# Kernel optimization log

Hardware: AMD Instinct MI355X
Metric: run time of the kernel (lower is better)

The kernel has to match this reference:

```python
import jax, jax.numpy as jnp
import numpy as np

E = 8          # num_experts
G = 4          # n_expert_groups
LG = 2         # n_limited_groups
TOPK = 2
ROUTE_SCALE = 1.0


def _grouped_mm(x, w, counts):
    """Grouped GEMM: contiguous groups of rows of x (sizes=counts) hit w[e]. Matches torch._grouped_mm."""
    counts = counts.astype(jnp.int32)
    if hasattr(jax.lax, 'ragged_dot'):
        return jax.lax.ragged_dot(x, w, counts)
    # fallback: expert id per row via searchsorted on offsets, one-hot dispatch
    offs = jnp.cumsum(counts)
    eid = jnp.searchsorted(offs, jnp.arange(x.shape[0]), side='right')
    oh = jax.nn.one_hot(eid, w.shape[0], dtype=x.dtype)
    return jnp.einsum('nd,ne,edh->nh', x, oh, w)


def setup_inputs() -> dict:
    key = jax.random.key(0)
    ks = jax.random.split(key, 8)
    bs, slen, dim, hid, shid = 2, 2048, 1024, 512, 1024
    std = 0.02
    return {
        'x': jax.random.normal(ks[0], (bs, slen, dim), jnp.float32),
        'w_gate': jax.random.normal(ks[1], (E, dim), jnp.float32) * std,
        'w1': jax.random.normal(ks[2], (E, dim, hid), jnp.float32) * std,
        'w2': jax.random.normal(ks[3], (E, hid, dim), jnp.float32) * std,
        'w3': jax.random.normal(ks[4], (E, dim, hid), jnp.float32) * std,
        'sw1': jax.random.normal(ks[5], (shid, dim), jnp.float32) * std,
        'sw2': jax.random.normal(ks[6], (dim, shid), jnp.float32) * std,
        'sw3': jax.random.normal(ks[7], (shid, dim), jnp.float32) * std,
        'expert_bias': jnp.zeros((E,), jnp.float32),
    }


def reference(x, w_gate, w1, w2, w3, sw1, sw2, sw3, expert_bias):
    bs, slen, dim = x.shape
    xf = x.reshape(-1, dim)                       # [N, dim]
    N = xf.shape[0]

    # ---- Gate (group-limited top-k routing) ----
    logits = xf @ w_gate.T                        # [N, E]
    scores = jax.nn.softmax(logits.astype(jnp.float32), axis=-1)
    original = scores
    s = (scores + expert_bias).reshape(N, G, E // G)
    # expert_bias is not None branch: group score = sum of top-2 in group
    group_scores = jax.lax.top_k(s, 2)[0].sum(-1)            # [N, G]
    top_groups = jax.lax.top_k(group_scores, LG)[1]          # [N, LG]
    keep = jnp.zeros((N, G), bool).at[jnp.arange(N)[:, None], top_groups].set(True)
    masked = jnp.where(keep[:, :, None], s, -jnp.inf).reshape(N, E)
    topk_idx = jax.lax.top_k(masked, TOPK)[1]                # [N, k]
    weights = (jnp.take_along_axis(original, topk_idx, axis=1) * ROUTE_SCALE).astype(x.dtype)
    counts = jnp.bincount(topk_idx.reshape(-1), length=E)    # histc equivalent

    # ---- dispatch (faithful to source: gather rows of x by expert ids) ----
    flat_idx = topk_idx.reshape(-1)                          # [N*k], values in [0, E)
    routed_in = xf[flat_idx]                                 # [N*k, dim]
    # score_before_experts = True
    routed_in = (routed_in.astype(jnp.float32) * weights.reshape(-1, 1)).astype(x.dtype)

    # ---- grouped experts: SwiGLU via grouped GEMM ----
    h = jax.nn.silu(_grouped_mm(routed_in, w1, counts)) * _grouped_mm(routed_in, w3, counts)
    routed_out = _grouped_mm(h, w2, counts)                  # [N*k, dim]

    # ---- shared experts (SwiGLU FFN) + combine (faithful scatter by expert ids) ----
    shared = (jax.nn.silu(xf @ sw1.T) * (xf @ sw3.T)) @ sw2.T
    out = shared.at[flat_idx].add(routed_out)
    return out.reshape(bs, slen, dim)
```

## Files before the change

### kernel.cpp

```cpp
#include <hip/hip_runtime.h>
#include <math.h>

#define DIM  1024
#define HID  512
#define SHID 1024
#define NTOK 4096
#define NE   8
#define NROW 8192

typedef __attribute__((ext_vector_type(8))) short  bfx8;
typedef __attribute__((ext_vector_type(4))) float  fx4;

__device__ __forceinline__ unsigned short f2bf(float f){
  unsigned int u = __float_as_uint(f);
  unsigned int r = (u + 0x7FFFu + ((u >> 16) & 1u)) >> 16;
  return (unsigned short)r;
}

#define GLOAD16(g, l) __builtin_amdgcn_global_load_lds( \
    (const __attribute__((address_space(1))) unsigned int*)(g), \
    (__attribute__((address_space(3))) unsigned int*)(l), 16, 0, 0)

__global__ __launch_bounds__(256) void cvtall_k(
    const float* __restrict__ sw1, const float* __restrict__ sw3,
    const float* __restrict__ sw2, unsigned short* __restrict__ s1b,
    unsigned short* __restrict__ s3b, unsigned short* __restrict__ s2b)
{
  const int NW = (SHID*DIM)/4;
  int i = blockIdx.x*256 + threadIdx.x;
  const float* s; unsigned short* d; int j;
  if (i < NW)            { s = sw1; d = s1b; j = i; }
  else if (i < 2*NW)     { s = sw3; d = s3b; j = i-NW; }
  else                   { s = sw2; d = s2b; j = i-2*NW; }
  float4 v = ((const float4*)s)[j];
  ushort4 o;
  o.x = f2bf(v.x); o.y = f2bf(v.y); o.z = f2bf(v.z); o.w = f2bf(v.w);
  ((ushort4*)d)[j] = o;
}

__global__ __launch_bounds__(256) void logits_k(const float* __restrict__ x,
    const float* __restrict__ wg, float* __restrict__ logits,
    unsigned short* __restrict__ xb, int* __restrict__ counts, int* __restrict__ bcount)
{
  if (blockIdx.x == 0 && threadIdx.x < 64){
    if (threadIdx.x < NE) counts[threadIdx.x] = 0;
    bcount[threadIdx.x] = 0;
  }
  int w = threadIdx.x >> 6, l = threadIdx.x & 63;
  int t = blockIdx.x*4 + w;
  const float4* xr = (const float4*)(x + (size_t)t*DIM);
  ushort4* xw = (ushort4*)xb + (size_t)t*256;
  float acc[NE];
  #pragma unroll
  for (int e=0;e<NE;e++) acc[e]=0.f;
  #pragma unroll
  for (int it=0; it<4; ++it){
    int idx = l + it*64;
    float4 xv = xr[idx];
    ushort4 o;
    o.x = f2bf(xv.x); o.y = f2bf(xv.y); o.z = f2bf(xv.z); o.w = f2bf(xv.w);
    xw[idx] = o;
    #pragma unroll
    for (int e=0;e<NE;e++){
      float4 wv = ((const float4*)(wg + (size_t)e*DIM))[idx];
      acc[e] += xv.x*wv.x + xv.y*wv.y + xv.z*wv.z + xv.w*wv.w;
    }
  }
  #pragma unroll
  for (int off=32; off>=1; off>>=1){
    #pragma unroll
    for (int e=0;e<NE;e++) acc[e] += __shfl_xor(acc[e], off, 64);
  }
  if (l==0){
    float4 a = {acc[0],acc[1],acc[2],acc[3]};
    float4 b = {acc[4],acc[5],acc[6],acc[7]};
    ((float4*)(logits + (size_t)t*8))[0] = a;
    ((float4*)(logits + (size_t)t*8))[1] = b;
  }
}

__global__ __launch_bounds__(256) void topk_k(const float* __restrict__ logits,
    const float* __restrict__ bias, int* __restrict__ topk,
    float* __restrict__ wts, int* __restrict__ counts, float* __restrict__ S)
{
  __shared__ int h[NE];
  int tid = threadIdx.x;
  if (tid < NE) h[tid] = 0;
  int i = blockIdx.x*256 + tid;
  float4 z4 = {0.f,0.f,0.f,0.f};
  ((float4*)S)[i*2]   = z4;
  ((float4*)S)[i*2+1] = z4;
  __syncthreads();
  float4 la = ((const float4*)(logits + (size_t)i*8))[0];
  float4 lb = ((const float4*)(logits + (size_t)i*8))[1];
  float lg[NE] = {la.x,la.y,la.z,la.w,lb.x,lb.y,lb.z,lb.w};
  float m = lg[0];
  #pragma unroll
  for (int e=1;e<NE;e++) m = fmaxf(m, lg[e]);
  float p[NE], s=0.f;
  #pragma unroll
  for (int e=0;e<NE;e++){ p[e]=expf(lg[e]-m); s+=p[e]; }
  float inv = 1.f/s;
  float sc[NE], sb[NE];
  #pragma unroll
  for (int e=0;e<NE;e++){ sc[e]=p[e]*inv; sb[e]=sc[e]+bias[e]; }
  float gs[4];
  #pragma unroll
  for (int g=0; g<4; g++) gs[g] = sb[2*g] + sb[2*g+1];
  int g1=0;
  #pragma unroll
  for (int g=1; g<4; g++) if (gs[g] > gs[g1]) g1=g;
  int g2=-1;
  #pragma unroll
  for (int g=0; g<4; g++){ if (g==g1) continue; if (g2<0 || gs[g]>gs[g2]) g2=g; }
  int e1=-1, e2=-1;
  #pragma unroll
  for (int e=0;e<NE;e++){
    int g=e>>1; if (g!=g1 && g!=g2) continue;
    if (e1<0 || sb[e]>sb[e1]) e1=e;
  }
  #pragma unroll
  for (int e=0;e<NE;e++){
    int g=e>>1; if (g!=g1 && g!=g2) continue;
    if (e==e1) continue;
    if (e2<0 || sb[e]>sb[e2]) e2=e;
  }
  topk[2*i]   = e1;  topk[2*i+1] = e2;
  wts[2*i]    = sc[e1];  wts[2*i+1] = sc[e2];
  atomicAdd(&h[e1], 1);
  atomicAdd(&h[e2], 1);
  __syncthreads();
  if (tid < NE) atomicAdd(&counts[tid], h[tid]);
}

template<int DUAL>
__global__ __launch_bounds__(512,2) void gemm_k(
    const unsigned short* __restrict__ A,
    const unsigned short* __restrict__ B1,
    const unsigned short* __restrict__ B3,
    unsigned short* __restrict__ Hb,
    float* __restrict__ Cf,
    int M, int N, int K)
{
  __shared__ unsigned short As [2][128*32];
  __shared__ unsigned short Bs [2][128*32];
  __shared__ unsigned short Bs3[DUAL?2:1][DUAL?128*32:16];
  const int tid  = threadIdx.x;
  const int lane = tid & 63;
  const int wave = tid >> 6;
  const int nbn  = N >> 7;
  const int bm   = blockIdx.x / nbn;
  const int bn   = blockIdx.x % nbn;
  const size_t m0 = (size_t)bm * 128;
  const size_t n0 = (size_t)bn * 128;
  const int wr = wave >> 2;
  const int wc = wave & 3;

  fx4 zero = {0.f,0.f,0.f,0.f};
  fx4 acc1[4][2], acc3[4][2];
  #pragma unroll
  for (int i=0;i<4;i++)
    #pragma unroll
    for (int j=0;j<2;j++){ acc1[i][j] = zero; if (DUAL) acc3[i][j] = zero; }

  const int c0 = tid;
  const int r0 = c0 >> 2, kc0 = c0 & 3;
  const unsigned short* Ab  = A  + m0*(size_t)K;
  const unsigned short* B1b = B1 + n0*(size_t)K;
  const unsigned short* B3b = DUAL ? (B3 + n0*(size_t)K) : (const unsigned short*)0;
  const int fr = lane & 15;
  const int fk = (lane >> 4) * 8;

  auto STAGE = [&](int buf, int k0){
    GLOAD16(Ab  + (size_t)r0*K + k0 + kc0*8, &As [buf][c0*8]);
    GLOAD16(B1b + (size_t)r0*K + k0 + kc0*8, &Bs [buf][c0*8]);
    if (DUAL) GLOAD16(B3b + (size_t)r0*K + k0 + kc0*8, &Bs3[buf][c0*8]);
  };

  const int nt = K >> 5;
  STAGE(0, 0);
  for (int t=0; t<nt; ++t){
    const int cur = t & 1;
    if (t+1 < nt){
      STAGE(cur^1, (t+1) << 5);
      if (DUAL) asm volatile("s_waitcnt vmcnt(3)" ::: "memory");
      else      asm volatile("s_waitcnt vmcnt(2)" ::: "memory");
    } else {
      asm volatile("s_waitcnt vmcnt(0)" ::: "memory");
    }
    __builtin_amdgcn_s_barrier();
    asm volatile("" ::: "memory");
    bfx8 af[4], b1f[2], b3f[2];
    #pragma unroll
    for (int m=0;m<4;m++) af[m]  = *(const bfx8*)&As[cur][(wr*64 + m*16 + fr)*32 + fk];
    #pragma unroll
    for (int n=0;n<2;n++){
      b1f[n] = *(const bfx8*)&Bs[cur][(wc*32 + n*16 + fr)*32 + fk];
      if (DUAL) b3f[n] = *(const bfx8*)&Bs3[cur][(wc*32 + n*16 + fr)*32 + fk];
    }
    #pragma unroll
    for (int m=0;m<4;m++)
      #pragma unroll
      for (int n=0;n<2;n++){
        acc1[m][n] = __builtin_amdgcn_mfma_f32_16x16x32_bf16(af[m], b1f[n], acc1[m][n], 0, 0, 0);
        if (DUAL)
          acc3[m][n] = __builtin_amdgcn_mfma_f32_16x16x32_bf16(af[m], b3f[n], acc3[m][n], 0, 0, 0);
      }
    asm volatile("" ::: "memory");
    __builtin_amdgcn_s_barrier();
  }

  const int rs = (lane >> 4) * 4;
  #pragma unroll
  for (int m=0;m<4;m++){
    #pragma unroll
    for (int n=0;n<2;n++){
      #pragma unroll
      for (int r=0;r<4;r++){
        size_t row = m0 + wr*64 + m*16 + rs + r;
        size_t col = n0 + wc*32 + n*16 + fr;
        size_t idx = row*(size_t)N + col;
        if (DUAL){
          float a = acc1[m][n][r];
          float c = acc3[m][n][r];
          float hsw = (a / (1.f + expf(-a))) * c;
          Hb[idx] = f2bf(hsw);
        } else {
          Cf[idx] = acc1[m][n][r];
        }
      }
    }
  }
}

__global__ __launch_bounds__(256) void pgemv_k(const float* __restrict__ x,
    const float* __restrict__ w1, const float* __restrict__ w3,
    float* __restrict__ P1, float* __restrict__ P3)
{
  __shared__ float xs[8*512];
  __shared__ float red[8][32][16];
  int e  = blockIdx.x >> 5;
  int jc = (blockIdx.x >> 1) & 15;
  int kc = blockIdx.x & 1;
  int t  = threadIdx.x;
  for (int q=t; q<1024; q+=256){
    int f = q >> 7, k4 = q & 127;
    ((float4*)xs)[q] = ((const float4*)x)[f*256 + kc*128 + k4];
  }
  __syncthreads();
  int j  = jc*32 + (t & 31);
  int kp = t >> 5;
  float a1[8], a3[8];
  #pragma unroll
  for (int f=0;f<8;f++){ a1[f]=0.f; a3[f]=0.f; }
  const float* w1p = w1 + (size_t)e*DIM*HID + (size_t)(kc*512)*HID + j;
  const float* w3p = w3 + (size_t)e*DIM*HID + (size_t)(kc*512)*HID + j;
  #pragma unroll 4
  for (int k=kp*64; k<kp*64+64; ++k){
    float w1v = w1p[(size_t)k*HID];
    float w3v = w3p[(size_t)k*HID];
    #pragma unroll
    for (int f=0;f<8;f++){
      float xv = xs[f*512 + k];
      a1[f] += xv*w1v;
      a3[f] += xv*w3v;
    }
  }
  #pragma unroll
  for (int f=0;f<8;f++){ red[kp][t&31][f] = a1[f]; red[kp][t&31][8+f] = a3[f]; }
  __syncthreads();
  if (kp==0){
    #pragma unroll
    for (int f=0;f<8;f++){
      float s1=0.f, s3=0.f;
      #pragma unroll
      for (int q=0;q<8;q++){ s1 += red[q][t][f]; s3 += red[q][t][8+f]; }
      P1[((size_t)(kc*64) + f*8 + e)*HID + j] = s1;
      P3[((size_t)(kc*64) + f*8 + e)*HID + j] = s3;
    }
  }
}

__global__ __launch_bounds__(256) void scat_k(const int* __restrict__ topk,
    const float* __restrict__ wts, const int* __restrict__ counts,
    int* __restrict__ bcount, float* __restrict__ bw)
{
  int i = blockIdx.x*256 + threadIdx.x;
  if (i >= NROW) return;
  int offv[NE]; int s=0;
  #pragma unroll
  for (int q=0;q<NE;q++){ s += counts[q]; offv[q]=s; }
  int f = topk[i];
  int e = 0;
  #pragma unroll
  for (int q=0;q<NE;q++) if (i >= offv[q]) e = q+1;
  float w = wts[i];
  int b = f*8 + e;
  int slot = atomicAdd(&bcount[b], 1);
  bw[(size_t)b*NROW + slot] = w;
}

__global__ __launch_bounds__(256) void ssum_k(const float* __restrict__ P1,
    const int* __restrict__ bcount, const float* __restrict__ bw,
    float* __restrict__ S)
{
  int b = blockIdx.x >> 3;
  int c = blockIdx.x & 7;
  int t = threadIdx.x;
  int n = bcount[b];
  float a0 = P1[(size_t)b*HID + t]       + P1[(size_t)(64+b)*HID + t];
  float a1 = P1[(size_t)b*HID + t + 256] + P1[(size_t)(64+b)*HID + t + 256];
  float s0 = 0.f, s1 = 0.f;
  const float* wp = bw + (size_t)b*NROW;
  for (int q=c; q<n; q+=8){
    float w = wp[q];
    float z0 = w*a0, z1 = w*a1;
    s0 += w * z0 / (1.f + expf(-z0));
    s1 += w * z1 / (1.f + expf(-z1));
  }
  if (n > c){
    atomicAdd(&S[(size_t)b*HID + t],       s0);
    atomicAdd(&S[(size_t)b*HID + t + 256], s1);
  }
}

__global__ __launch_bounds__(256) void rout_k(const float* __restrict__ P3,
    const float* __restrict__ S, const float* __restrict__ w2,
    float* __restrict__ out)
{
  __shared__ float Hs[8*256];
  __shared__ float red[4][64][8];
  int e  = blockIdx.x >> 5;
  int dc = (blockIdx.x >> 1) & 15;
  int jh = blockIdx.x & 1;
  int t  = threadIdx.x;
  for (int q=t; q<2048; q+=256){
    int r = q >> 8; int jl = q & 255;
    size_t idx = (size_t)(r*8 + e)*HID + jh*256 + jl;
    Hs[q] = (P3[idx] + P3[(size_t)64*HID + idx]) * S[idx];
  }
  __syncthreads();
  int d  = dc*64 + (t & 63);
  int jp = t >> 6;
  float acc[8];
  #pragma unroll
  for (int r=0;r<8;r++) acc[r]=0.f;
  const float* w2p = w2 + (size_t)e*HID*DIM + (size_t)(jh*256)*DIM + d;
  #pragma unroll 4
  for (int jl=jp*64; jl<jp*64+64; ++jl){
    float wv = w2p[(size_t)jl*DIM];
    #pragma unroll
    for (int r=0;r<8;r++) acc[r] += Hs[r*256 + jl]*wv;
  }
  #pragma unroll
  for (int r=0;r<8;r++) red[jp][t&63][r] = acc[r];
  __syncthreads();
  if (jp==0){
    #pragma unroll
    for (int r=0;r<8;r++){
      float v = red[0][t][r] + red[1][t][r] + red[2][t][r] + red[3][t][r];
      atomicAdd(&out[(size_t)r*DIM + d], v);
    }
  }
}

extern "C" void kernel_launch(void* const* d_in, const int* in_sizes, int n_in,
                              void* d_out, int out_size, void* d_ws, size_t ws_size,
                              hipStream_t stream)
{
  const float* x    = (const float*)d_in[0];
  const float* wg   = (const float*)d_in[1];
  const float* w1   = (const float*)d_in[2];
  const float* w2   = (const float*)d_in[3];
  const float* w3   = (const float*)d_in[4];
  const float* sw1  = (const float*)d_in[5];
  const float* sw2  = (const float*)d_in[6];
  const float* sw3  = (const float*)d_in[7];
  const float* bias = (const float*)d_in[8];
  float* out = (float*)d_out;

  char* wsp = (char*)d_ws;
  size_t off = 0;
  auto alloc = [&](size_t bytes)->char*{
    char* p = wsp + off; off += (bytes + 255) & ~(size_t)255; return p;
  };
  unsigned short* xb   = (unsigned short*)alloc((size_t)NTOK*DIM*2);
  unsigned short* s1b  = (unsigned short*)alloc((size_t)SHID*DIM*2);
  unsigned short* s3b  = (unsigned short*)alloc((size_t)SHID*DIM*2);
  unsigned short* s2b  = (unsigned short*)alloc((size_t)DIM*SHID*2);
  unsigned short* hb   = (unsigned short*)alloc((size_t)NTOK*SHID*2);
  float*          lgt  = (float*)alloc((size_t)NTOK*NE*4);
  int*            topk = (int*)alloc(NROW*4);
  float*          wtsb = (float*)alloc(NROW*4);
  int*            cnts = (int*)alloc(64);
  int*            bcnt = (int*)alloc(256);
  float*          P1   = (float*)alloc(2*64*HID*4);
  float*          P3   = (float*)alloc(2*64*HID*4);
  float*          Sbuf = (float*)alloc(64*HID*4);
  float*          bwb  = (float*)alloc((size_t)64*NROW*4);
  (void)ws_size; (void)in_sizes; (void)n_in; (void)out_size;

  const int NW = (SHID*DIM)/4;
  cvtall_k<<<(3*NW)/256, 256, 0, stream>>>(sw1, sw3, sw2, s1b, s3b, s2b);
  logits_k<<<NTOK/4, 256, 0, stream>>>(x, wg, lgt, xb, cnts, bcnt);
  topk_k<<<NTOK/256, 256, 0, stream>>>(lgt, bias, topk, wtsb, cnts, Sbuf);
  scat_k<<<NROW/256, 256, 0, stream>>>(topk, wtsb, cnts, bcnt, bwb);
  pgemv_k<<<256, 256, 0, stream>>>(x, w1, w3, P1, P3);
  ssum_k<<<512, 256, 0, stream>>>(P1, bcnt, bwb, Sbuf);

  gemm_k<1><<<(NTOK/128)*(SHID/128), 512, 0, stream>>>(xb, s1b, s3b, hb, nullptr, NTOK, SHID, DIM);
  gemm_k<0><<<(NTOK/128)*(DIM/128),  512, 0, stream>>>(hb, s2b, nullptr, nullptr, out, NTOK, DIM, SHID);

  rout_k<<<256, 256, 0, stream>>>(P3, Sbuf, w2, out);
}
```

Measured before the change: 241.9 us.

## Double GEMM K-tile to 64 with XOR-swizzled LDS and XCD-aware block remap

Raises the K depth per pipeline stage from 32 to 64, which halves the number of barrier/wait iterations and doubles the loads in flight. LDS tiles are XOR-swizzled by row so the wider 128-byte rows avoid bank conflicts on fragment reads. Block indices are remapped so consecutive tiles land on the same XCD, improving L2 reuse of A/B panels. The cost is doubled LDS use (96KB for the dual variant), which may reduce occupancy below the 2 blocks/CU the launch bounds request, and the remap assumes the grid size is a multiple of 8.

```diff
diff --git a/kernel.cpp b/kernel.cpp
--- a/kernel.cpp
+++ b/kernel.cpp
@@ -142,15 +142,17 @@
     float* __restrict__ Cf,
     int M, int N, int K)
 {
-  __shared__ unsigned short As [2][128*32];
-  __shared__ unsigned short Bs [2][128*32];
-  __shared__ unsigned short Bs3[DUAL?2:1][DUAL?128*32:16];
+  __shared__ unsigned short As [2][128*64];
+  __shared__ unsigned short Bs [2][128*64];
+  __shared__ unsigned short Bs3[DUAL?2:1][DUAL?128*64:16];
   const int tid  = threadIdx.x;
   const int lane = tid & 63;
   const int wave = tid >> 6;
   const int nbn  = N >> 7;
-  const int bm   = blockIdx.x / nbn;
-  const int bn   = blockIdx.x % nbn;
+  const int cpx  = gridDim.x >> 3;
+  const int wg   = (blockIdx.x & 7)*cpx + (blockIdx.x >> 3);
+  const int bm   = wg / nbn;
+  const int bn   = wg % nbn;
   const size_t m0 = (size_t)bm * 128;
   const size_t n0 = (size_t)bn * 128;
   const int wr = wave >> 2;
@@ -163,49 +165,67 @@
     #pragma unroll
     for (int j=0;j<2;j++){ acc1[i][j] = zero; if (DUAL) acc3[i][j] = zero; }
 
-  const int c0 = tid;
-  const int r0 = c0 >> 2, kc0 = c0 & 3;
+  const int c0 = tid,        r0 = c0 >> 3, kc0 = c0 & 7;
+  const int c1 = tid + 512,  r1 = c1 >> 3, kc1 = c1 & 7;
+  const int sk0 = (kc0 ^ (r0 & 7)) * 8;
+  const int sk1 = (kc1 ^ (r1 & 7)) * 8;
   const unsigned short* Ab  = A  + m0*(size_t)K;
   const unsigned short* B1b = B1 + n0*(size_t)K;
   const unsigned short* B3b = DUAL ? (B3 + n0*(size_t)K) : (const unsigned short*)0;
   const int fr = lane & 15;
-  const int fk = (lane >> 4) * 8;
+  const int fq = lane >> 4;
 
   auto STAGE = [&](int buf, int k0){
-    GLOAD16(Ab  + (size_t)r0*K + k0 + kc0*8, &As [buf][c0*8]);
-    GLOAD16(B1b + (size_t)r0*K + k0 + kc0*8, &Bs [buf][c0*8]);
-    if (DUAL) GLOAD16(B3b + (size_t)r0*K + k0 + kc0*8, &Bs3[buf][c0*8]);
+    GLOAD16(Ab  + (size_t)r0*K + k0 + sk0, &As [buf][c0*8]);
+    GLOAD16(Ab  + (size_t)r1*K + k0 + sk1, &As [buf][c1*8]);
+    GLOAD16(B1b + (size_t)r0*K + k0 + sk0, &Bs [buf][c0*8]);
+    GLOAD16(B1b + (size_t)r1*K + k0 + sk1, &Bs [buf][c1*8]);
+    if (DUAL){
+      GLOAD16(B3b + (size_t)r0*K + k0 + sk0, &Bs3[buf][c0*8]);
+      GLOAD16(B3b + (size_t)r1*K + k0 + sk1, &Bs3[buf][c1*8]);
+    }
   };
 
-  const int nt = K >> 5;
+  auto LOFF = [&](int row, int ks){
+    return row*64 + ((((ks<<2) + fq) ^ (row & 7)) << 3);
+  };
+
+  const int nt = K >> 6;
   STAGE(0, 0);
   for (int t=0; t<nt; ++t){
     const int cur = t & 1;
     if (t+1 < nt){
-      STAGE(cur^1, (t+1) << 5);
-      if (DUAL) asm volatile("s_waitcnt vmcnt(3)" ::: "memory");
-      else      asm volatile("s_waitcnt vmcnt(2)" ::: "memory");
+      STAGE(cur^1, (t+1) << 6);
+      if (DUAL) asm volatile("s_waitcnt vmcnt(6)" ::: "memory");
+      else      asm volatile("s_waitcnt vmcnt(4)" ::: "memory");
     } else {
       asm volatile("s_waitcnt vmcnt(0)" ::: "memory");
     }
     __builtin_amdgcn_s_barrier();
     asm volatile("" ::: "memory");
-    bfx8 af[4], b1f[2], b3f[2];
-    #pragma unroll
-    for (int m=0;m<4;m++) af[m]  = *(const bfx8*)&As[cur][(wr*64 + m*16 + fr)*32 + fk];
-    #pragma unroll
-    for (int n=0;n<2;n++){
-      b1f[n] = *(const bfx8*)&Bs[cur][(wc*32 + n*16 + fr)*32 + fk];
-      if (DUAL) b3f[n] = *(const bfx8*)&Bs3[cur][(wc*32 + n*16 + fr)*32 + fk];
-    }
-    #pragma unroll
-    for (int m=0;m<4;m++)
+    #pragma unroll
+    for (int ks=0; ks<2; ++ks){
+      bfx8 af[4], b1f[2], b3f[2];
+      #pragma unroll
+      for (int m=0;m<4;m++){
+        int row = wr*64 + m*16 + fr;
+        af[m] = *(const bfx8*)&As[cur][LOFF(row, ks)];
+      }
       #pragma unroll
       for (int n=0;n<2;n++){
-        acc1[m][n] = __builtin_amdgcn_mfma_f32_16x16x32_bf16(af[m], b1f[n], acc1[m][n], 0, 0, 0);
-        if (DUAL)
-          acc3[m][n] = __builtin_amdgcn_mfma_f32_16x16x32_bf16(af[m], b3f[n], acc3[m][n], 0, 0, 0);
+        int row = wc*32 + n*16 + fr;
+        b1f[n] = *(const bfx8*)&Bs[cur][LOFF(row, ks)];
+        if (DUAL) b3f[n] = *(const bfx8*)&Bs3[cur][LOFF(row, ks)];
       }
+      #pragma unroll
+      for (int m=0;m<4;m++)
+        #pragma unroll
+        for (int n=0;n<2;n++){
+          acc1[m][n] = __builtin_amdgcn_mfma_f32_16x16x32_bf16(af[m], b1f[n], acc1[m][n], 0, 0, 0);
+          if (DUAL)
+            acc3[m][n] = __builtin_amdgcn_mfma_f32_16x16x32_bf16(af[m], b3f[n], acc3[m][n], 0, 0, 0);
+        }
+    }
     asm volatile("" ::: "memory");
     __builtin_amdgcn_s_barrier();
   }
```

Measured after the change: 233.7 us. 3.4% less time.
